# Optimization experiments

Hardware: AMD Instinct MI355X
Metric: run time of the kernel (lower is better)

Reference implementation:

```python
import jax, jax.numpy as jnp
import numpy as np

_LN_EPS = 1e-5

def _gelu(x):
    return jax.nn.gelu(x, approximate=False)

def _layernorm(x, g, b):
    mu = x.mean(-1, keepdims=True)
    var = ((x - mu) ** 2).mean(-1, keepdims=True)
    return (x - mu) * jax.lax.rsqrt(var + _LN_EPS) * g + b

def setup_inputs() -> dict:
    key = jax.random.key(0)
    ks = jax.random.split(key, 8)
    B, S, D = 4, 2048, 1024
    N_IN, N_PROC, D_R = 8192, 4096, 256
    s = 0.02
    return {
        "x": jax.random.normal(ks[0], (B, S, D), jnp.float32),
        "W1": jax.random.normal(ks[1], (2 * D_R, D), jnp.float32) * s,
        "b1": jnp.zeros((2 * D_R,), jnp.float32),
        "ln_g": jnp.ones((2 * D_R,), jnp.float32),
        "ln_b": jnp.zeros((2 * D_R,), jnp.float32),
        "W2": jax.random.normal(ks[2], (D_R, 2 * D_R), jnp.float32) * s,
        "b2": jnp.zeros((D_R,), jnp.float32),
        "neuron_keys": jax.random.normal(ks[3], (N_IN, D_R), jnp.float32) * s,
        "input_patterns": jax.random.normal(ks[4], (N_IN, D), jnp.float32) * s,
        "process_weights": jax.random.normal(ks[5], (N_PROC, N_IN), jnp.float32) * s,
        "process_outputs": jax.random.normal(ks[6], (N_PROC, D), jnp.float32) * s,
        "k_input": 4096,
        "k_process": 2048,
    }

def reference(x, W1, b1, ln_g, ln_b, W2, b2, neuron_keys, input_patterns,
              process_weights, process_outputs, k_input, k_process):
    d_routing = neuron_keys.shape[1]
    # --- Global router: sequence max-pool context -> query -> top-k input neurons
    gc = x.max(axis=1)                                   # [B, D]
    h = _layernorm(_gelu(gc @ W1.T + b1), ln_g, ln_b)    # [B, 2*d_r]
    query = h @ W2.T + b2                                # [B, d_r]
    logits = (query @ neuron_keys.T) / jnp.sqrt(jnp.asarray(d_routing, x.dtype))  # [B, N_in]
    _, input_idx = jax.lax.top_k(logits, k_input)        # [B, k_in]
    # --- Input neuron activations, gather selected ones
    input_acts = _gelu(jnp.einsum('bsd,nd->bsn', x, input_patterns))   # [B,S,N_in]
    sel_acts = jnp.take_along_axis(input_acts, input_idx[:, None, :], axis=2)  # [B,S,k_in]
    # --- Per-batch gather of process weight columns, process activations
    W_sel = jnp.take(process_weights, input_idx, axis=1)               # [N_proc,B,k_in]
    proc_acts = _gelu(jnp.einsum('bsk,pbk->bsp', sel_acts, W_sel))     # [B,S,N_proc]
    scores = proc_acts.mean(axis=1)                                    # [B,N_proc]
    _, proc_idx = jax.lax.top_k(scores, k_process)                     # [B,k_proc]
    sel_proc = jnp.take_along_axis(proc_acts, proc_idx[:, None, :], axis=2)  # [B,S,k_proc]
    out_w = process_outputs[proc_idx]                                  # [B,k_proc,D]
    return jnp.einsum('bsk,bkd->bsd', sel_proc, out_w)                 # [B,S,D]
```

## Files before the change

kernel.cpp:

```cpp
#include <hip/hip_runtime.h>
#include <cstdint>

#define B_    4
#define S_    2048
#define D_    1024
#define NIN   8192
#define NPROC 4096
#define DR    256
#define DR2   512
#define KIN   4096
#define KPROC 2048

typedef _Float16 v8h  __attribute__((ext_vector_type(8)));
typedef _Float16 v4h  __attribute__((ext_vector_type(4)));
typedef float    v4f  __attribute__((ext_vector_type(4)));
typedef float    v16f __attribute__((ext_vector_type(16)));

__device__ __forceinline__ float geluf(float v) {
    return 0.5f * v * (1.0f + erff(v * 0.70710678f));
}

__device__ __forceinline__ void cp16(void* lds, const void* g) {
    __builtin_amdgcn_global_load_lds(
        (const __attribute__((address_space(1))) unsigned int*)g,
        (__attribute__((address_space(3))) unsigned int*)lds, 16, 0, 0);
}

__global__ void k_conv_x16(const float* __restrict__ x, _Float16* __restrict__ x16, int n4) {
    int i = blockIdx.x * 256 + threadIdx.x;
    if (i < n4) {
        float4 v = ((const float4*)x)[i];
        v4h h = { (_Float16)v.x, (_Float16)v.y, (_Float16)v.z, (_Float16)v.w };
        ((v4h*)x16)[i] = h;
    }
}

__global__ void k_conv_split(const float* __restrict__ p, _Float16* __restrict__ ph,
                             _Float16* __restrict__ pl, int n) {
    int i = blockIdx.x * 256 + threadIdx.x;
    if (i < n) {
        float v = p[i];
        _Float16 h = (_Float16)v;
        ph[i] = h;
        pl[i] = (_Float16)(v - (float)h);
    }
}

__global__ void k_max1(const float* __restrict__ x, float* __restrict__ pmax) {
    int d = blockIdx.x * 256 + threadIdx.x;
    int chunk = blockIdx.y;
    int b = blockIdx.z;
    const float* base = x + ((size_t)b * S_ + chunk * 128) * D_ + d;
    float m = -3.4e38f;
    for (int s = 0; s < 128; s++) m = fmaxf(m, base[(size_t)s * D_]);
    pmax[((size_t)b * 16 + chunk) * D_ + d] = m;
}

__global__ void k_max2(const float* __restrict__ pmax, double* __restrict__ gc64) {
    int d = blockIdx.x * 256 + threadIdx.x;
    int b = blockIdx.y;
    float m = -3.4e38f;
    for (int c = 0; c < 16; c++) m = fmaxf(m, pmax[((size_t)b * 16 + c) * D_ + d]);
    gc64[(size_t)b * D_ + d] = (double)m;
}

__global__ __launch_bounds__(256) void k_router1(
    const double* __restrict__ gc64, const float* __restrict__ W1, const float* __restrict__ b1,
    double* __restrict__ hpre)
{
    int wave = threadIdx.x >> 6, lane = threadIdx.x & 63;
    int j = blockIdx.x * 4 + wave;
    int b = blockIdx.y;
    const double* g = gc64 + (size_t)b * D_;
    const float* w = W1 + (size_t)j * D_;
    double acc = 0.0;
    for (int d = lane; d < D_; d += 64) acc += g[d] * (double)w[d];
#pragma unroll
    for (int o = 32; o > 0; o >>= 1) acc += __shfl_xor(acc, o, 64);
    if (lane == 0) {
        double z = acc + (double)b1[j];
        hpre[(size_t)b * DR2 + j] = 0.5 * z * (1.0 + erf(z * 0.7071067811865475244));
    }
}

__global__ __launch_bounds__(512) void k_router2(
    const double* __restrict__ hpre, const float* __restrict__ lng, const float* __restrict__ lnb,
    const float* __restrict__ W2, const float* __restrict__ b2, double* __restrict__ qs)
{
    __shared__ double sh[DR2];
    __shared__ double red[DR2];
    int b = blockIdx.x, j = threadIdx.x;
    double ge = hpre[(size_t)b * DR2 + j];
    sh[j] = ge; red[j] = ge;
    __syncthreads();
    for (int s = 256; s > 0; s >>= 1) { if (j < s) red[j] += red[j + s]; __syncthreads(); }
    double mu = red[0] / 512.0;
    __syncthreads();
    double dv = ge - mu;
    red[j] = dv * dv;
    __syncthreads();
    for (int s = 256; s > 0; s >>= 1) { if (j < s) red[j] += red[j + s]; __syncthreads(); }
    double rs = 1.0 / sqrt(red[0] / 512.0 + 1e-5);
    __syncthreads();
    sh[j] = dv * rs * (double)lng[j] + (double)lnb[j];
    __syncthreads();
    if (j < DR) {
        double q = (double)b2[j];
        const float* w2r = W2 + (size_t)j * DR2;
        for (int t = 0; t < DR2; t++) q += sh[t] * (double)w2r[t];
        qs[(size_t)b * DR + j] = q;
    }
}

__global__ __launch_bounds__(256) void k_router3(
    const double* __restrict__ qs, const float* __restrict__ keys, double* __restrict__ logits)
{
    int wave = threadIdx.x >> 6, lane = threadIdx.x & 63;
    int n = blockIdx.x * 4 + wave;
    int b = blockIdx.y;
    const double* q = qs + (size_t)b * DR;
    const float* kr = keys + (size_t)n * DR;
    double acc = 0.0;
#pragma unroll
    for (int t = 0; t < 4; t++) {
        int d = lane + t * 64;
        acc += q[d] * (double)kr[d];
    }
#pragma unroll
    for (int o = 32; o > 0; o >>= 1) acc += __shfl_xor(acc, o, 64);
    if (lane == 0) logits[(size_t)b * NIN + n] = acc * 0.0625;
}

template<int N, int K>
__global__ __launch_bounds__(1024) void k_topk(const double* __restrict__ vals, int* __restrict__ outIdx) {
    __shared__ unsigned long long keys[N];
    int b = blockIdx.x, tid = threadIdx.x;
    for (int i = tid; i < N; i += 1024) {
        float v = (float)vals[(size_t)b * N + i];
        unsigned int u = __float_as_uint(v);
        u = (u & 0x80000000u) ? ~u : (u | 0x80000000u);
        keys[i] = ((unsigned long long)u << 32) | (unsigned int)(~i);
    }
    __syncthreads();
    for (int k = 2; k <= N; k <<= 1)
        for (int j = k >> 1; j > 0; j >>= 1) {
            for (int i = tid; i < N; i += 1024) {
                int l = i ^ j;
                if (l > i) {
                    unsigned long long a = keys[i], c = keys[l];
                    bool up = ((i & k) == 0);
                    if ((a < c) == up) { keys[i] = c; keys[l] = a; }
                }
            }
            __syncthreads();
        }
    for (int i = tid; i < K; i += 1024)
        outIdx[(size_t)b * K + i] = (int)(~(unsigned int)keys[i]);
}

__device__ __forceinline__ void dev_gatherW(const float* __restrict__ pw, const int* __restrict__ iidx,
                                            _Float16* __restrict__ Wh, _Float16* __restrict__ Wl,
                                            int p, int b, size_t bstride) {
    const float* row = pw + (size_t)p * NIN;
    const int* ix = iidx + (size_t)b * KIN;
    _Float16* wh = Wh + bstride + (size_t)p * KIN;
    _Float16* wl = Wl + bstride + (size_t)p * KIN;
    for (int j = threadIdx.x; j < KIN; j += 256) {
        float w = row[ix[j]];
        _Float16 h = (_Float16)w;
        wh[j] = h;
        wl[j] = (_Float16)(w - (float)h);
    }
}

__global__ void k_gatherSP(const _Float16* __restrict__ acts16, const int* __restrict__ pidx,
                           _Float16* __restrict__ sp) {
    int s = blockIdx.x, b = blockIdx.y;
    const _Float16* arow = acts16 + ((size_t)b * S_ + s) * NPROC;
    _Float16* orow = sp + ((size_t)b * S_ + s) * KPROC;
    const int* pi = pidx + (size_t)b * KPROC;
    for (int k = threadIdx.x; k < KPROC; k += 256) orow[k] = arow[pi[k]];
}

__global__ void k_gatherWoT(const _Float16* __restrict__ pout16, const int* __restrict__ pidx,
                            _Float16* __restrict__ woT) {
    __shared__ _Float16 t[64][65];
    int k0 = blockIdx.x * 64, d0 = blockIdx.y * 64, b = blockIdx.z;
    const int* pi = pidx + (size_t)b * KPROC;
    for (int i = threadIdx.x; i < 4096; i += 256) {
        int kk = i >> 6, dd = i & 63;
        t[kk][dd] = pout16[(size_t)pi[k0 + kk] * D_ + d0 + dd];
    }
    __syncthreads();
    for (int i = threadIdx.x; i < 4096; i += 256) {
        int dd = i >> 6, kk = i & 63;
        woT[((size_t)b * D_ + d0 + dd) * KPROC + k0 + kk] = t[kk][dd];
    }
}


__device__ __forceinline__ void dev_gemmD(
    const _Float16* __restrict__ x16, const _Float16* __restrict__ ph, const _Float16* __restrict__ pl,
    const int* __restrict__ iidx, _Float16* __restrict__ a16,
    _Float16* tA, _Float16* tBh, _Float16* tBl, int bx, int by, int b)
{
    const int m0 = bx * 256, n0 = by * 128;
    const int tid = threadIdx.x, lane = tid & 63;
    const int wave = tid >> 6, wrow = wave >> 1, wcol = wave & 1;
    const int srow = tid >> 2, spart = tid & 3;
    const int spe = spart ^ ((srow >> 1) & 3);

    const _Float16* as0 = x16 + ((size_t)b * S_ + m0 + srow) * D_ + spe * 8;
    int r0 = iidx[(size_t)b * KIN + n0 + srow];
    int r1 = iidx[(size_t)b * KIN + n0 + srow + 64];
    const _Float16* bh0 = ph + (size_t)r0 * D_ + spe * 8;
    const _Float16* bh1 = ph + (size_t)r1 * D_ + spe * 8;
    const _Float16* bl0 = pl + (size_t)r0 * D_ + spe * 8;
    const _Float16* bl1 = pl + (size_t)r1 * D_ + spe * 8;

    v16f acc[4][2];
#pragma unroll
    for (int i = 0; i < 4; i++)
#pragma unroll
        for (int j = 0; j < 2; j++) acc[i][j] = (v16f)(0.0f);

    const int lrow = lane & 31, lhi = lane >> 5;
    const int swz = (lane >> 1) & 3;
    const int abase = (wrow * 128 + lrow) * 32;
    const int bbase = (wcol * 64 + lrow) * 32;

    for (int kt = 0; kt < D_; kt += 32) {
        __syncthreads();
        cp16(&tA[tid * 8],        as0 + kt);
        cp16(&tA[2048 + tid * 8], as0 + (size_t)64  * D_ + kt);
        cp16(&tA[4096 + tid * 8], as0 + (size_t)128 * D_ + kt);
        cp16(&tA[6144 + tid * 8], as0 + (size_t)192 * D_ + kt);
        cp16(&tBh[tid * 8],        bh0 + kt);
        cp16(&tBh[2048 + tid * 8], bh1 + kt);
        cp16(&tBl[tid * 8],        bl0 + kt);
        cp16(&tBl[2048 + tid * 8], bl1 + kt);
        asm volatile("s_waitcnt vmcnt(0)" ::: "memory");
        __syncthreads();
#pragma unroll
        for (int kw = 0; kw < 2; kw++) {
            const int ch = ((kw * 2 + lhi) ^ swz) * 8;
            v8h af[4], fh[2], fl[2];
#pragma unroll
            for (int mi = 0; mi < 4; mi++) af[mi] = *(const v8h*)&tA[abase + mi * 1024 + ch];
#pragma unroll
            for (int nj = 0; nj < 2; nj++) {
                fh[nj] = *(const v8h*)&tBh[bbase + nj * 1024 + ch];
                fl[nj] = *(const v8h*)&tBl[bbase + nj * 1024 + ch];
            }
#pragma unroll
            for (int mi = 0; mi < 4; mi++)
#pragma unroll
                for (int nj = 0; nj < 2; nj++) {
                    acc[mi][nj] = __builtin_amdgcn_mfma_f32_32x32x16_f16(af[mi], fh[nj], acc[mi][nj], 0, 0, 0);
                    acc[mi][nj] = __builtin_amdgcn_mfma_f32_32x32x16_f16(af[mi], fl[nj], acc[mi][nj], 0, 0, 0);
                }
        }
    }
#pragma unroll
    for (int mi = 0; mi < 4; mi++)
#pragma unroll
        for (int nj = 0; nj < 2; nj++)
#pragma unroll
            for (int r = 0; r < 16; r++) {
                int row = (r & 3) + 8 * (r >> 2) + 4 * lhi;
                float gv = geluf(acc[mi][nj][r]);
                a16[((size_t)b * S_ + m0 + wrow * 128 + mi * 32 + row) * (size_t)KIN
                    + n0 + wcol * 64 + nj * 32 + lrow] = (_Float16)gv;
            }
}

__global__ __launch_bounds__(256, 2) void k_gemmD(
    const _Float16* __restrict__ x16, const _Float16* __restrict__ ph, const _Float16* __restrict__ pl,
    const int* __restrict__ iidx, _Float16* __restrict__ a16)
{
    __shared__ _Float16 tA[8192], tBh[4096], tBl[4096];
    dev_gemmD(x16, ph, pl, iidx, a16, tA, tBh, tBl, blockIdx.x, blockIdx.y, blockIdx.z);
}

__global__ __launch_bounds__(256, 2) void k_fusedDW(
    const _Float16* __restrict__ x16, const _Float16* __restrict__ ph, const _Float16* __restrict__ pl,
    const int* __restrict__ iidx, _Float16* __restrict__ a16,
    const float* __restrict__ pw, _Float16* __restrict__ Wh, _Float16* __restrict__ Wl, size_t wstride)
{
    __shared__ _Float16 tA[8192], tBh[4096], tBl[4096];
    if (blockIdx.z >= 4) {
        int idx = (blockIdx.z - 4) * 256 + blockIdx.y * 8 + blockIdx.x;
        int p = idx >> 2, b = idx & 3;
        dev_gatherW(pw, iidx, Wh, Wl, p, b, (size_t)b * wstride);
        return;
    }
    dev_gemmD(x16, ph, pl, iidx, a16, tA, tBh, tBl, blockIdx.x, blockIdx.y, blockIdx.z);
}

__global__ void k_gatherW(const float* __restrict__ pw, const int* __restrict__ iidx,
                          _Float16* __restrict__ Wh, _Float16* __restrict__ Wl,
                          int b_base, size_t wstride) {
    dev_gatherW(pw, iidx, Wh, Wl, blockIdx.x, b_base + blockIdx.y, (size_t)blockIdx.y * wstride);
}

__global__ __launch_bounds__(256, 2) void k_gemmE(
    const _Float16* __restrict__ a16, const _Float16* __restrict__ Wh, const _Float16* __restrict__ Wl,
    _Float16* __restrict__ acts16, double* __restrict__ scores, int b_base, size_t wstride)
{
    const int b = b_base + blockIdx.z;
    const int m0 = blockIdx.x * 256, n0 = blockIdx.y * 128;
    __shared__ _Float16 tA[8192], tBh[4096], tBl[4096];
    const int tid = threadIdx.x, lane = tid & 63;
    const int wave = tid >> 6, wrow = wave >> 1, wcol = wave & 1;
    const int srow = tid >> 2, spart = tid & 3;
    const int spe = spart ^ ((srow >> 1) & 3);

    const _Float16* as0 = a16 + ((size_t)b * S_ + m0 + srow) * (size_t)KIN + spe * 8;
    const _Float16* whB = Wh + (size_t)blockIdx.z * wstride;
    const _Float16* wlB = Wl + (size_t)blockIdx.z * wstride;
    const _Float16* bh0 = whB + (size_t)(n0 + srow) * KIN + spe * 8;
    const _Float16* bh1 = bh0 + (size_t)64 * KIN;
    const _Float16* bl0 = wlB + (size_t)(n0 + srow) * KIN + spe * 8;
    const _Float16* bl1 = bl0 + (size_t)64 * KIN;

    v16f acc[4][2];
#pragma unroll
    for (int i = 0; i < 4; i++)
#pragma unroll
        for (int j = 0; j < 2; j++) acc[i][j] = (v16f)(0.0f);

    const int lrow = lane & 31, lhi = lane >> 5;
    const int swz = (lane >> 1) & 3;
    const int abase = (wrow * 128 + lrow) * 32;
    const int bbase = (wcol * 64 + lrow) * 32;

    for (int kt = 0; kt < KIN; kt += 32) {
        __syncthreads();
        cp16(&tA[tid * 8],        as0 + kt);
        cp16(&tA[2048 + tid * 8], as0 + (size_t)64  * KIN + kt);
        cp16(&tA[4096 + tid * 8], as0 + (size_t)128 * KIN + kt);
        cp16(&tA[6144 + tid * 8], as0 + (size_t)192 * KIN + kt);
        cp16(&tBh[tid * 8],        bh0 + kt);
        cp16(&tBh[2048 + tid * 8], bh1 + kt);
        cp16(&tBl[tid * 8],        bl0 + kt);
        cp16(&tBl[2048 + tid * 8], bl1 + kt);
        asm volatile("s_waitcnt vmcnt(0)" ::: "memory");
        __syncthreads();
#pragma unroll
        for (int kw = 0; kw < 2; kw++) {
            const int ch = ((kw * 2 + lhi) ^ swz) * 8;
            v8h af[4], fh[2], fl[2];
#pragma unroll
            for (int mi = 0; mi < 4; mi++) af[mi] = *(const v8h*)&tA[abase + mi * 1024 + ch];
#pragma unroll
            for (int nj = 0; nj < 2; nj++) {
                fh[nj] = *(const v8h*)&tBh[bbase + nj * 1024 + ch];
                fl[nj] = *(const v8h*)&tBl[bbase + nj * 1024 + ch];
            }
#pragma unroll
            for (int mi = 0; mi < 4; mi++)
#pragma unroll
                for (int nj = 0; nj < 2; nj++) {
                    acc[mi][nj] = __builtin_amdgcn_mfma_f32_32x32x16_f16(af[mi], fh[nj], acc[mi][nj], 0, 0, 0);
                    acc[mi][nj] = __builtin_amdgcn_mfma_f32_32x32x16_f16(af[mi], fl[nj], acc[mi][nj], 0, 0, 0);
                }
        }
    }
    float psum[2] = {0.f, 0.f};
#pragma unroll
    for (int mi = 0; mi < 4; mi++)
#pragma unroll
        for (int nj = 0; nj < 2; nj++)
#pragma unroll
            for (int r = 0; r < 16; r++) {
                int row = (r & 3) + 8 * (r >> 2) + 4 * lhi;
                float gv = geluf(acc[mi][nj][r]);
                acts16[((size_t)b * S_ + m0 + wrow * 128 + mi * 32 + row) * (size_t)NPROC
                       + n0 + wcol * 64 + nj * 32 + lrow] = (_Float16)gv;
                psum[nj] += gv;
            }
#pragma unroll
    for (int nj = 0; nj < 2; nj++) {
        float s = psum[nj];
        s += __shfl_xor(s, 32, 64);
        if (lhi == 0)
            atomicAdd(&scores[(size_t)b * NPROC + n0 + wcol * 64 + nj * 32 + lrow], (double)s);
    }
}

__global__ __launch_bounds__(256, 2) void k_gemmF(
    const _Float16* __restrict__ sp, const _Float16* __restrict__ woT, float* __restrict__ out)
{
    const int b = blockIdx.z;
    const int m0 = blockIdx.x * 256, n0 = blockIdx.y * 128;
    __shared__ _Float16 tA[8192], tB[4096];
    const int tid = threadIdx.x, lane = tid & 63;
    const int wave = tid >> 6, wrow = wave >> 1, wcol = wave & 1;
    const int srow = tid >> 2, spart = tid & 3;
    const int spe = spart ^ ((srow >> 1) & 3);

    const _Float16* as0 = sp + ((size_t)b * S_ + m0 + srow) * (size_t)KPROC + spe * 8;
    const _Float16* bs0 = woT + ((size_t)b * D_ + n0 + srow) * (size_t)KPROC + spe * 8;
    const _Float16* bs1 = bs0 + (size_t)64 * KPROC;

    v16f acc[4][2];
#pragma unroll
    for (int i = 0; i < 4; i++)
#pragma unroll
        for (int j = 0; j < 2; j++) acc[i][j] = (v16f)(0.0f);

    const int lrow = lane & 31, lhi = lane >> 5;
    const int swz = (lane >> 1) & 3;
    const int abase = (wrow * 128 + lrow) * 32;
    const int bbase = (wcol * 64 + lrow) * 32;

    for (int kt = 0; kt < KPROC; kt += 32) {
        __syncthreads();
        cp16(&tA[tid * 8],        as0 + kt);
        cp16(&tA[2048 + tid * 8], as0 + (size_t)64  * KPROC + kt);
        cp16(&tA[4096 + tid * 8], as0 + (size_t)128 * KPROC + kt);
        cp16(&tA[6144 + tid * 8], as0 + (size_t)192 * KPROC + kt);
        cp16(&tB[tid * 8],        bs0 + kt);
        cp16(&tB[2048 + tid * 8], bs1 + kt);
        asm volatile("s_waitcnt vmcnt(0)" ::: "memory");
        __syncthreads();
#pragma unroll
        for (int kw = 0; kw < 2; kw++) {
            const int ch = ((kw * 2 + lhi) ^ swz) * 8;
            v8h af[4], bf[2];
#pragma unroll
            for (int mi = 0; mi < 4; mi++) af[mi] = *(const v8h*)&tA[abase + mi * 1024 + ch];
#pragma unroll
            for (int nj = 0; nj < 2; nj++) bf[nj] = *(const v8h*)&tB[bbase + nj * 1024 + ch];
#pragma unroll
            for (int mi = 0; mi < 4; mi++)
#pragma unroll
                for (int nj = 0; nj < 2; nj++)
                    acc[mi][nj] = __builtin_amdgcn_mfma_f32_32x32x16_f16(af[mi], bf[nj], acc[mi][nj], 0, 0, 0);
        }
    }
#pragma unroll
    for (int mi = 0; mi < 4; mi++)
#pragma unroll
        for (int nj = 0; nj < 2; nj++)
#pragma unroll
            for (int r = 0; r < 16; r++) {
                int row = (r & 3) + 8 * (r >> 2) + 4 * lhi;
                out[((size_t)b * S_ + m0 + wrow * 128 + mi * 32 + row) * (size_t)D_
                    + n0 + wcol * 64 + nj * 32 + lrow] = acc[mi][nj][r];
            }
}

extern "C" void kernel_launch(void* const* d_in, const int* in_sizes, int n_in,
                              void* d_out, int out_size, void* d_ws, size_t ws_size,
                              hipStream_t stream) {
    const float* x    = (const float*)d_in[0];
    const float* W1   = (const float*)d_in[1];
    const float* b1   = (const float*)d_in[2];
    const float* lng  = (const float*)d_in[3];
    const float* lnb  = (const float*)d_in[4];
    const float* W2   = (const float*)d_in[5];
    const float* b2   = (const float*)d_in[6];
    const float* keys = (const float*)d_in[7];
    const float* patt = (const float*)d_in[8];
    const float* pw   = (const float*)d_in[9];
    const float* pout = (const float*)d_in[10];
    (void)in_sizes; (void)n_in; (void)out_size;

    char* w = (char*)d_ws;
    size_t off = 0;
    auto alloc = [&](size_t bytes) -> void* {
        void* p = w + off;
        off += (bytes + 255) & ~(size_t)255;
        return p;
    };
    double* gc64   = (double*)alloc((size_t)B_ * D_ * 8);
    float*  pmax   = (float*) alloc((size_t)B_ * 16 * D_ * 4);
    double* logits = (double*)alloc((size_t)B_ * NIN * 8);
    double* scores = (double*)alloc((size_t)B_ * NPROC * 8);
    double* hpre   = (double*)alloc((size_t)B_ * DR2 * 8);
    double* qs     = (double*)alloc((size_t)B_ * DR * 8);
    int*    iidx   = (int*)   alloc((size_t)B_ * KIN * 4);
    int*    pidx   = (int*)   alloc((size_t)B_ * KPROC * 4);
    _Float16* a16    = (_Float16*)alloc((size_t)B_ * S_ * KIN * 2);
    _Float16* acts16 = (_Float16*)alloc((size_t)B_ * S_ * NPROC * 2);
    _Float16* pout16 = (_Float16*)alloc((size_t)NPROC * D_ * 2);
    char* u1 = (char*)alloc((size_t)67108864);
    _Float16* x16 = (_Float16*)u1;
    _Float16* ph  = (_Float16*)(u1 + 16777216);
    _Float16* pl  = (_Float16*)(u1 + 33554432);
    _Float16* WhT = (_Float16*)u1;
    _Float16* WlT = (_Float16*)(u1 + 33554432);
    _Float16* sp  = (_Float16*)u1;
    _Float16* woT = (_Float16*)(u1 + 33554432);

    const size_t WSTRIDE = (size_t)NPROC * KIN;
    size_t off_before_fat = off;
    _Float16* WhA = (_Float16*)alloc((size_t)B_ * WSTRIDE * 2);
    _Float16* WlA = (_Float16*)alloc((size_t)B_ * WSTRIDE * 2);
    bool fat = (off <= ws_size);
    if (!fat) off = off_before_fat;

    hipMemsetAsync(scores, 0, (size_t)B_ * NPROC * 8, stream);

    k_conv_x16 <<<dim3((B_ * S_ * D_ / 4 + 255) / 256), 256, 0, stream>>>(x, x16, B_ * S_ * D_ / 4);
    k_conv_split<<<dim3((NIN * D_ + 255) / 256), 256, 0, stream>>>(patt, ph, pl, NIN * D_);
    k_conv_x16 <<<dim3((NPROC * D_ / 4 + 255) / 256), 256, 0, stream>>>(pout, pout16, NPROC * D_ / 4);

    k_max1<<<dim3(4, 16, 4), 256, 0, stream>>>(x, pmax);
    k_max2<<<dim3(4, 4), 256, 0, stream>>>(pmax, gc64);
    k_router1<<<dim3(128, 4), 256, 0, stream>>>(gc64, W1, b1, hpre);
    k_router2<<<dim3(4), 512, 0, stream>>>(hpre, lng, lnb, W2, b2, qs);
    k_router3<<<dim3(2048, 4), 256, 0, stream>>>(qs, keys, logits);
    k_topk<NIN, KIN><<<dim3(4), 1024, 0, stream>>>(logits, iidx);

    if (fat) {
        k_fusedDW<<<dim3(8, 32, 68), 256, 0, stream>>>(x16, ph, pl, iidx, a16, pw, WhA, WlA, WSTRIDE);
        k_gemmE<<<dim3(8, 32, 4), 256, 0, stream>>>(a16, WhA, WlA, acts16, scores, 0, WSTRIDE);
    } else {
        k_gemmD<<<dim3(8, 32, 4), 256, 0, stream>>>(x16, ph, pl, iidx, a16);
        for (int b = 0; b < 4; b++) {
            k_gatherW<<<dim3(NPROC, 1), 256, 0, stream>>>(pw, iidx, WhT, WlT, b, 0);
            k_gemmE<<<dim3(8, 32, 1), 256, 0, stream>>>(a16, WhT, WlT, acts16, scores, b, 0);
        }
    }

    k_topk<NPROC, KPROC><<<dim3(4), 1024, 0, stream>>>(scores, pidx);
    k_gatherSP<<<dim3(S_, 4), 256, 0, stream>>>(acts16, pidx, sp);
    k_gatherWoT<<<dim3(KPROC / 64, D_ / 64, 4), 256, 0, stream>>>(pout16, pidx, woT);
    k_gemmF<<<dim3(8, 8, 4), 256, 0, stream>>>(sp, woT, (float*)d_out);
}
```

Measured before the change: 1.642 ms.

## Double-buffer LDS tiles with prefetch two stages ahead in all three GEMMs

Replaces the single-buffer load-wait-compute loop in the three MFMA GEMM kernels with a two-buffer pipeline. Tiles for step t+2 are issued while step t computes, using partial vmcnt waits, explicit barriers, sched_barrier fences and raised wave priority around the MFMA block. This is meant to hide global-to-LDS latency behind matrix math. It doubles LDS use per block (64KB for D/E), which may limit occupancy under launch_bounds(256,2).

```diff
diff --git a/kernel.cpp b/kernel.cpp
--- a/kernel.cpp
+++ b/kernel.cpp
@@ -229,37 +229,57 @@
     const int abase = (wrow * 128 + lrow) * 32;
     const int bbase = (wcol * 64 + lrow) * 32;
 
-    for (int kt = 0; kt < D_; kt += 32) {
-        __syncthreads();
-        cp16(&tA[tid * 8],        as0 + kt);
-        cp16(&tA[2048 + tid * 8], as0 + (size_t)64  * D_ + kt);
-        cp16(&tA[4096 + tid * 8], as0 + (size_t)128 * D_ + kt);
-        cp16(&tA[6144 + tid * 8], as0 + (size_t)192 * D_ + kt);
-        cp16(&tBh[tid * 8],        bh0 + kt);
-        cp16(&tBh[2048 + tid * 8], bh1 + kt);
-        cp16(&tBl[tid * 8],        bl0 + kt);
-        cp16(&tBl[2048 + tid * 8], bl1 + kt);
-        asm volatile("s_waitcnt vmcnt(0)" ::: "memory");
-        __syncthreads();
+    auto STAGE = [&](int buf, int kt) {
+        const int oA = buf * 8192, oB = buf * 4096;
+        cp16(&tA[oA + tid * 8],        as0 + kt);
+        cp16(&tA[oA + 2048 + tid * 8], as0 + (size_t)64 * D_ + kt);
+        cp16(&tA[oA + 4096 + tid * 8], as0 + (size_t)128 * D_ + kt);
+        cp16(&tA[oA + 6144 + tid * 8], as0 + (size_t)192 * D_ + kt);
+        cp16(&tBh[oB + tid * 8],        bh0 + kt);
+        cp16(&tBh[oB + 2048 + tid * 8], bh1 + kt);
+        cp16(&tBl[oB + tid * 8],        bl0 + kt);
+        cp16(&tBl[oB + 2048 + tid * 8], bl1 + kt);
+    };
+
+    const int nt = D_ / 32;
+    STAGE(0, 0);
+    STAGE(1, 32);
+
+    for (int t = 0; t < nt; t++) {
+        const int oA = (t & 1) * 8192, oB = (t & 1) * 4096;
+        if (t + 1 < nt) { asm volatile("s_waitcnt vmcnt(8)" ::: "memory"); }
+        else            { asm volatile("s_waitcnt vmcnt(0)" ::: "memory"); }
+        __builtin_amdgcn_s_barrier();
+        __builtin_amdgcn_sched_barrier(0);
+        v8h af[4][2], fh[2][2], fl[2][2];
 #pragma unroll
         for (int kw = 0; kw < 2; kw++) {
             const int ch = ((kw * 2 + lhi) ^ swz) * 8;
-            v8h af[4], fh[2], fl[2];
-#pragma unroll
-            for (int mi = 0; mi < 4; mi++) af[mi] = *(const v8h*)&tA[abase + mi * 1024 + ch];
+#pragma unroll
+            for (int mi = 0; mi < 4; mi++) af[mi][kw] = *(const v8h*)&tA[oA + abase + mi * 1024 + ch];
 #pragma unroll
             for (int nj = 0; nj < 2; nj++) {
-                fh[nj] = *(const v8h*)&tBh[bbase + nj * 1024 + ch];
-                fl[nj] = *(const v8h*)&tBl[bbase + nj * 1024 + ch];
+                fh[nj][kw] = *(const v8h*)&tBh[oB + bbase + nj * 1024 + ch];
+                fl[nj][kw] = *(const v8h*)&tBl[oB + bbase + nj * 1024 + ch];
             }
+        }
+        asm volatile("s_waitcnt lgkmcnt(0)" ::: "memory");
+        __builtin_amdgcn_sched_barrier(0);
+        __builtin_amdgcn_s_barrier();
+        __builtin_amdgcn_sched_barrier(0);
+        if (t + 2 < nt) STAGE(t & 1, (t + 2) * 32);
+        __builtin_amdgcn_sched_barrier(0);
+        __builtin_amdgcn_s_setprio(1);
+#pragma unroll
+        for (int kw = 0; kw < 2; kw++)
 #pragma unroll
             for (int mi = 0; mi < 4; mi++)
 #pragma unroll
                 for (int nj = 0; nj < 2; nj++) {
-                    acc[mi][nj] = __builtin_amdgcn_mfma_f32_32x32x16_f16(af[mi], fh[nj], acc[mi][nj], 0, 0, 0);
-                    acc[mi][nj] = __builtin_amdgcn_mfma_f32_32x32x16_f16(af[mi], fl[nj], acc[mi][nj], 0, 0, 0);
+                    acc[mi][nj] = __builtin_amdgcn_mfma_f32_32x32x16_f16(af[mi][kw], fh[nj][kw], acc[mi][nj], 0, 0, 0);
+                    acc[mi][nj] = __builtin_amdgcn_mfma_f32_32x32x16_f16(af[mi][kw], fl[nj][kw], acc[mi][nj], 0, 0, 0);
                 }
-        }
+        __builtin_amdgcn_s_setprio(0);
     }
 #pragma unroll
     for (int mi = 0; mi < 4; mi++)
@@ -278,7 +298,7 @@
     const _Float16* __restrict__ x16, const _Float16* __restrict__ ph, const _Float16* __restrict__ pl,
     const int* __restrict__ iidx, _Float16* __restrict__ a16)
 {
-    __shared__ _Float16 tA[8192], tBh[4096], tBl[4096];
+    __shared__ _Float16 tA[16384], tBh[8192], tBl[8192];
     dev_gemmD(x16, ph, pl, iidx, a16, tA, tBh, tBl, blockIdx.x, blockIdx.y, blockIdx.z);
 }
 
@@ -287,7 +307,7 @@
     const int* __restrict__ iidx, _Float16* __restrict__ a16,
     const float* __restrict__ pw, _Float16* __restrict__ Wh, _Float16* __restrict__ Wl, size_t wstride)
 {
-    __shared__ _Float16 tA[8192], tBh[4096], tBl[4096];
+    __shared__ _Float16 tA[16384], tBh[8192], tBl[8192];
     if (blockIdx.z >= 4) {
         int idx = (blockIdx.z - 4) * 256 + blockIdx.y * 8 + blockIdx.x;
         int p = idx >> 2, b = idx & 3;
@@ -309,7 +329,7 @@
 {
     const int b = b_base + blockIdx.z;
     const int m0 = blockIdx.x * 256, n0 = blockIdx.y * 128;
-    __shared__ _Float16 tA[8192], tBh[4096], tBl[4096];
+    __shared__ _Float16 tA[16384], tBh[8192], tBl[8192];
     const int tid = threadIdx.x, lane = tid & 63;
     const int wave = tid >> 6, wrow = wave >> 1, wcol = wave & 1;
     const int srow = tid >> 2, spart = tid & 3;
@@ -334,37 +354,57 @@
     const int abase = (wrow * 128 + lrow) * 32;
     const int bbase = (wcol * 64 + lrow) * 32;
 
-    for (int kt = 0; kt < KIN; kt += 32) {
-        __syncthreads();
-        cp16(&tA[tid * 8],        as0 + kt);
-        cp16(&tA[2048 + tid * 8], as0 + (size_t)64  * KIN + kt);
-        cp16(&tA[4096 + tid * 8], as0 + (size_t)128 * KIN + kt);
-        cp16(&tA[6144 + tid * 8], as0 + (size_t)192 * KIN + kt);
-        cp16(&tBh[tid * 8],        bh0 + kt);
-        cp16(&tBh[2048 + tid * 8], bh1 + kt);
-        cp16(&tBl[tid * 8],        bl0 + kt);
-        cp16(&tBl[2048 + tid * 8], bl1 + kt);
-        asm volatile("s_waitcnt vmcnt(0)" ::: "memory");
-        __syncthreads();
+    auto STAGE = [&](int buf, int kt) {
+        const int oA = buf * 8192, oB = buf * 4096;
+        cp16(&tA[oA + tid * 8],        as0 + kt);
+        cp16(&tA[oA + 2048 + tid * 8], as0 + (size_t)64 * KIN + kt);
+        cp16(&tA[oA + 4096 + tid * 8], as0 + (size_t)128 * KIN + kt);
+        cp16(&tA[oA + 6144 + tid * 8], as0 + (size_t)192 * KIN + kt);
+        cp16(&tBh[oB + tid * 8],        bh0 + kt);
+        cp16(&tBh[oB + 2048 + tid * 8], bh1 + kt);
+        cp16(&tBl[oB + tid * 8],        bl0 + kt);
+        cp16(&tBl[oB + 2048 + tid * 8], bl1 + kt);
+    };
+
+    const int nt = KIN / 32;
+    STAGE(0, 0);
+    STAGE(1, 32);
+
+    for (int t = 0; t < nt; t++) {
+        const int oA = (t & 1) * 8192, oB = (t & 1) * 4096;
+        if (t + 1 < nt) { asm volatile("s_waitcnt vmcnt(8)" ::: "memory"); }
+        else            { asm volatile("s_waitcnt vmcnt(0)" ::: "memory"); }
+        __builtin_amdgcn_s_barrier();
+        __builtin_amdgcn_sched_barrier(0);
+        v8h af[4][2], fh[2][2], fl[2][2];
 #pragma unroll
         for (int kw = 0; kw < 2; kw++) {
             const int ch = ((kw * 2 + lhi) ^ swz) * 8;
-            v8h af[4], fh[2], fl[2];
-#pragma unroll
-            for (int mi = 0; mi < 4; mi++) af[mi] = *(const v8h*)&tA[abase + mi * 1024 + ch];
+#pragma unroll
+            for (int mi = 0; mi < 4; mi++) af[mi][kw] = *(const v8h*)&tA[oA + abase + mi * 1024 + ch];
 #pragma unroll
             for (int nj = 0; nj < 2; nj++) {
-                fh[nj] = *(const v8h*)&tBh[bbase + nj * 1024 + ch];
-                fl[nj] = *(const v8h*)&tBl[bbase + nj * 1024 + ch];
+                fh[nj][kw] = *(const v8h*)&tBh[oB + bbase + nj * 1024 + ch];
+                fl[nj][kw] = *(const v8h*)&tBl[oB + bbase + nj * 1024 + ch];
             }
+        }
+        asm volatile("s_waitcnt lgkmcnt(0)" ::: "memory");
+        __builtin_amdgcn_sched_barrier(0);
+        __builtin_amdgcn_s_barrier();
+        __builtin_amdgcn_sched_barrier(0);
+        if (t + 2 < nt) STAGE(t & 1, (t + 2) * 32);
+        __builtin_amdgcn_sched_barrier(0);
+        __builtin_amdgcn_s_setprio(1);
+#pragma unroll
+        for (int kw = 0; kw < 2; kw++)
 #pragma unroll
             for (int mi = 0; mi < 4; mi++)
 #pragma unroll
                 for (int nj = 0; nj < 2; nj++) {
-                    acc[mi][nj] = __builtin_amdgcn_mfma_f32_32x32x16_f16(af[mi], fh[nj], acc[mi][nj], 0, 0, 0);
-                    acc[mi][nj] = __builtin_amdgcn_mfma_f32_32x32x16_f16(af[mi], fl[nj], acc[mi][nj], 0, 0, 0);
+                    acc[mi][nj] = __builtin_amdgcn_mfma_f32_32x32x16_f16(af[mi][kw], fh[nj][kw], acc[mi][nj], 0, 0, 0);
+                    acc[mi][nj] = __builtin_amdgcn_mfma_f32_32x32x16_f16(af[mi][kw], fl[nj][kw], acc[mi][nj], 0, 0, 0);
                 }
-        }
+        __builtin_amdgcn_s_setprio(0);
     }
     float psum[2] = {0.f, 0.f};
 #pragma unroll
@@ -393,7 +433,7 @@
 {
     const int b = blockIdx.z;
     const int m0 = blockIdx.x * 256, n0 = blockIdx.y * 128;
-    __shared__ _Float16 tA[8192], tB[4096];
+    __shared__ _Float16 tA[16384], tB[8192];
     const int tid = threadIdx.x, lane = tid & 63;
     const int wave = tid >> 6, wrow = wave >> 1, wcol = wave & 1;
     const int srow = tid >> 2, spart = tid & 3;
@@ -414,30 +454,50 @@
     const int abase = (wrow * 128 + lrow) * 32;
     const int bbase = (wcol * 64 + lrow) * 32;
 
-    for (int kt = 0; kt < KPROC; kt += 32) {
-        __syncthreads();
-        cp16(&tA[tid * 8],        as0 + kt);
-        cp16(&tA[2048 + tid * 8], as0 + (size_t)64  * KPROC + kt);
-        cp16(&tA[4096 + tid * 8], as0 + (size_t)128 * KPROC + kt);
-        cp16(&tA[6144 + tid * 8], as0 + (size_t)192 * KPROC + kt);
-        cp16(&tB[tid * 8],        bs0 + kt);
-        cp16(&tB[2048 + tid * 8], bs1 + kt);
-        asm volatile("s_waitcnt vmcnt(0)" ::: "memory");
-        __syncthreads();
+    auto STAGE = [&](int buf, int kt) {
+        const int oA = buf * 8192, oB = buf * 4096;
+        cp16(&tA[oA + tid * 8],        as0 + kt);
+        cp16(&tA[oA + 2048 + tid * 8], as0 + (size_t)64 * KPROC + kt);
+        cp16(&tA[oA + 4096 + tid * 8], as0 + (size_t)128 * KPROC + kt);
+        cp16(&tA[oA + 6144 + tid * 8], as0 + (size_t)192 * KPROC + kt);
+        cp16(&tB[oB + tid * 8],        bs0 + kt);
+        cp16(&tB[oB + 2048 + tid * 8], bs1 + kt);
+    };
+
+    const int nt = KPROC / 32;
+    STAGE(0, 0);
+    STAGE(1, 32);
+
+    for (int t = 0; t < nt; t++) {
+        const int oA = (t & 1) * 8192, oB = (t & 1) * 4096;
+        if (t + 1 < nt) { asm volatile("s_waitcnt vmcnt(6)" ::: "memory"); }
+        else            { asm volatile("s_waitcnt vmcnt(0)" ::: "memory"); }
+        __builtin_amdgcn_s_barrier();
+        __builtin_amdgcn_sched_barrier(0);
+        v8h af[4][2], bf[2][2];
 #pragma unroll
         for (int kw = 0; kw < 2; kw++) {
             const int ch = ((kw * 2 + lhi) ^ swz) * 8;
-            v8h af[4], bf[2];
-#pragma unroll
-            for (int mi = 0; mi < 4; mi++) af[mi] = *(const v8h*)&tA[abase + mi * 1024 + ch];
-#pragma unroll
-            for (int nj = 0; nj < 2; nj++) bf[nj] = *(const v8h*)&tB[bbase + nj * 1024 + ch];
+#pragma unroll
+            for (int mi = 0; mi < 4; mi++) af[mi][kw] = *(const v8h*)&tA[oA + abase + mi * 1024 + ch];
+#pragma unroll
+            for (int nj = 0; nj < 2; nj++) bf[nj][kw] = *(const v8h*)&tB[oB + bbase + nj * 1024 + ch];
+        }
+        asm volatile("s_waitcnt lgkmcnt(0)" ::: "memory");
+        __builtin_amdgcn_sched_barrier(0);
+        __builtin_amdgcn_s_barrier();
+        __builtin_amdgcn_sched_barrier(0);
+        if (t + 2 < nt) STAGE(t & 1, (t + 2) * 32);
+        __builtin_amdgcn_sched_barrier(0);
+        __builtin_amdgcn_s_setprio(1);
+#pragma unroll
+        for (int kw = 0; kw < 2; kw++)
 #pragma unroll
             for (int mi = 0; mi < 4; mi++)
 #pragma unroll
                 for (int nj = 0; nj < 2; nj++)
-                    acc[mi][nj] = __builtin_amdgcn_mfma_f32_32x32x16_f16(af[mi], bf[nj], acc[mi][nj], 0, 0, 0);
-        }
+                    acc[mi][nj] = __builtin_amdgcn_mfma_f32_32x32x16_f16(af[mi][kw], bf[nj][kw], acc[mi][nj], 0, 0, 0);
+        __builtin_amdgcn_s_setprio(0);
     }
 #pragma unroll
     for (int mi = 0; mi < 4; mi++)
```

New measurement: 1.495 ms. -8.9%, faster.
